# Performance work log

Hardware: AMD Instinct MI355X
Metric: run time of the kernel (lower is better)

The kernel has to match this reference:

```python
import jax, jax.numpy as jnp
import numpy as np
import math

B, S, D, H = 8, 512, 1024, 16
HD = D // H  # 64
FF = 4 * D
EPS = 1e-5


def setup_inputs() -> dict:
    key = jax.random.key(0)
    ks = jax.random.split(key, 12)
    sc = 0.02
    return {
        "x":   jax.random.normal(ks[0], (B, S, D), jnp.float32),
        "Wq":  jax.random.normal(ks[1], (H, D, HD), jnp.float32) * sc,
        "Wk":  jax.random.normal(ks[2], (H, D, HD), jnp.float32) * sc,
        "Wv":  jax.random.normal(ks[3], (H, D, HD), jnp.float32) * sc,
        "Wo":  jax.random.normal(ks[4], (D, D), jnp.float32) * sc,
        "bo":  jnp.zeros((D,), jnp.float32),
        "g1":  jnp.ones((D,), jnp.float32),
        "b1":  jnp.zeros((D,), jnp.float32),
        "g2":  jnp.ones((D,), jnp.float32),
        "b2":  jnp.zeros((D,), jnp.float32),
        "W1":  jax.random.normal(ks[5], (D, FF), jnp.float32) * sc,
        "bf1": jnp.zeros((FF,), jnp.float32),
        "W2":  jax.random.normal(ks[6], (FF, D), jnp.float32) * sc,
        "bf2": jnp.zeros((D,), jnp.float32),
    }


def _layernorm(x, gamma, beta):
    # biased variance, matches torch.var(correction=0)
    mean = jnp.mean(x, axis=-1, keepdims=True)
    var = jnp.mean((x - mean) ** 2, axis=-1, keepdims=True)
    return (x - mean) / jnp.sqrt(var + EPS) * gamma + beta


def _block(x, Wq, Wk, Wv, Wo, bo, g1, b1, g2, b2, W1, bf1, W2, bf2):
    h = _layernorm(x, g1, b1)
    # per-head projections (no bias): [B,H,S,HD]
    Q = jnp.einsum("bsd,hde->bhse", h, Wq)
    K = jnp.einsum("bsd,hde->bhse", h, Wk)
    V = jnp.einsum("bsd,hde->bhse", h, Wv)
    scores = jnp.einsum("bhse,bhte->bhst", Q, K) / math.sqrt(HD)
    causal = jnp.triu(jnp.ones((S, S), bool), k=1)  # upper-triangular masked
    scores = jnp.where(causal, jnp.float32(-1e10), scores)
    att = jax.nn.softmax(scores, axis=-1)  # dropout in eval mode = identity
    ctx = jnp.einsum("bhst,bhte->bhse", att, V)
    # concat heads in order -> [B,S,D]
    ctx = ctx.transpose(0, 2, 1, 3).reshape(B, S, D)
    attn_out = ctx @ Wo + bo
    cache = attn_out + x
    h2 = _layernorm(cache, g2, b2)
    ff = jax.nn.gelu(h2 @ W1 + bf1, approximate=False) @ W2 + bf2
    return ff + cache


def reference(x, Wq, Wk, Wv, Wo, bo, g1, b1, g2, b2, W1, bf1, W2, bf2):
    return _block(x, Wq, Wk, Wv, Wo, bo, g1, b1, g2, b2, W1, bf1, W2, bf2)
```

## Files before the change

### kernel.cpp

```cpp
#include <hip/hip_runtime.h>
#include <hip/hip_bf16.h>

typedef __hip_bfloat16 bf16;

#define B_   8
#define S_   512
#define D_   1024
#define H_   16
#define HD_  64
#define FF_  4096
#define ROWS (B_ * S_)

typedef __attribute__((ext_vector_type(8))) unsigned short u16x8;
typedef __attribute__((ext_vector_type(4))) float f32x4;

typedef __attribute__((address_space(1))) const unsigned int GU32;
typedef __attribute__((address_space(3))) unsigned int LU32;
__device__ __forceinline__ void gld16(const void* g, void* l) {
    __builtin_amdgcn_global_load_lds((GU32*)g, (LU32*)l, 16, 0, 0);
}

__device__ __forceinline__ float bf2f(unsigned short u) {
    union { unsigned int i; float f; } v; v.i = ((unsigned int)u) << 16; return v.f;
}
__device__ __forceinline__ unsigned short f2bfu(float f) {
    bf16 h = __float2bfloat16(f);
    return *reinterpret_cast<unsigned short*>(&h);
}
__device__ __forceinline__ float ldsel(const void* p, size_t i, bool f32) {
    return f32 ? ((const float*)p)[i]
               : __bfloat162float(((const bf16*)p)[i]);
}
__device__ __forceinline__ float gelu_exact(float x) {
    return 0.5f * x * (1.f + erff(x * 0.70710678118654752440f));
}

__device__ __forceinline__ void ln_body(const void* x, const void* gam,
                                        const void* bet, bf16* out,
                                        int row, bool xf32, bool pf32) {
    int tid = threadIdx.x;
    size_t rb = (size_t)row * D_;
    float v[4];
#pragma unroll
    for (int i = 0; i < 4; ++i) v[i] = ldsel(x, rb + tid + i * 256, xf32);
    float s  = v[0] + v[1] + v[2] + v[3];
    float s2 = v[0] * v[0] + v[1] * v[1] + v[2] * v[2] + v[3] * v[3];
#pragma unroll
    for (int off = 32; off > 0; off >>= 1) {
        s  += __shfl_down(s, off);
        s2 += __shfl_down(s2, off);
    }
    __shared__ float red[8];
    int wv = tid >> 6, ln = tid & 63;
    if (ln == 0) { red[wv] = s; red[4 + wv] = s2; }
    __syncthreads();
    s  = red[0] + red[1] + red[2] + red[3];
    s2 = red[4] + red[5] + red[6] + red[7];
    float mean = s * (1.f / 1024.f);
    float var  = s2 * (1.f / 1024.f) - mean * mean;
    float rstd = rsqrtf(var + 1e-5f);
#pragma unroll
    for (int i = 0; i < 4; ++i) {
        int c = tid + i * 256;
        float g = ldsel(gam, c, pf32), b = ldsel(bet, c, pf32);
        out[rb + c] = __float2bfloat16((v[i] - mean) * rstd * g + b);
    }
}

__device__ __forceinline__ void transpose_body(
    const void* src, bf16* dst, int bid, int N, int K, int sK, int sH, bool pf32) {
    int tilesN = N >> 6;
    int tn = bid % tilesN, tk = bid / tilesN;
    int n0 = tn * 64, k0 = tk * 64;
    __shared__ float T[64][65];
    int t = threadIdx.x;
    size_t headoff = (size_t)(n0 >> 6) * sH;
#pragma unroll
    for (int i = 0; i < 16; ++i) {
        int lin = t + i * 256;
        int kl = lin >> 6, nl = lin & 63;
        size_t e = headoff + (size_t)(k0 + kl) * sK + nl;
        T[kl][nl] = ldsel(src, e, pf32);
    }
    __syncthreads();
#pragma unroll
    for (int i = 0; i < 16; ++i) {
        int lin = t + i * 256;
        int nl = lin >> 6, kl = lin & 63;
        dst[(size_t)(n0 + nl) * K + k0 + kl] = __float2bfloat16(T[kl][nl]);
    }
}

__global__ __launch_bounds__(256) void transpose_kernel(
    const void* __restrict__ src, bf16* __restrict__ dst,
    int N, int K, int sK, int sH,
    const unsigned short* __restrict__ probe) {
    transpose_body(src, dst, blockIdx.x, N, K, sK, sH, probe[0] == 0);
}

__global__ __launch_bounds__(256) void prep1_kernel(
    const void* __restrict__ Wq, const void* __restrict__ Wk,
    const void* __restrict__ Wv, const void* __restrict__ Wo,
    const void* __restrict__ x, const void* __restrict__ g1,
    const void* __restrict__ b1,
    bf16* __restrict__ WqT, bf16* __restrict__ WoT, bf16* __restrict__ h,
    const unsigned short* __restrict__ probe) {
    bool pf32 = (probe[0] == 0);
    int bid = blockIdx.x;
    if (bid < 768) {
        int which = bid >> 8;
        const void* src = (which == 0) ? Wq : ((which == 1) ? Wk : Wv);
        transpose_body(src, WqT + (size_t)which * 1024 * 1024, bid & 255,
                       1024, 1024, HD_, D_ * HD_, pf32);
    } else if (bid < 1024) {
        transpose_body(Wo, WoT, bid - 768, 1024, 1024, 1024, 64, pf32);
    } else {
        ln_body(x, g1, b1, h, bid - 1024, pf32, pf32);
    }
}

__global__ __launch_bounds__(256) void prep2_kernel(
    const void* __restrict__ W1, const void* __restrict__ cache_,
    const void* __restrict__ g2, const void* __restrict__ b2,
    bf16* __restrict__ W1T, bf16* __restrict__ h2,
    const unsigned short* __restrict__ probe) {
    bool pf32 = (probe[0] == 0);
    int bid = blockIdx.x;
    if (bid < 1024) transpose_body(W1, W1T, bid, 4096, 1024, FF_, 64, pf32);
    else            ln_body(cache_, g2, b2, h2, bid - 1024, false, pf32);
}

template<int BN>
__global__ __launch_bounds__(256) void gemm_mfma(
    const bf16* __restrict__ A, const bf16* __restrict__ Bt,
    int K, int nSeg, int segShift, size_t segStride,
    const void* __restrict__ bias,
    const void* __restrict__ resid, int resid_ws,
    bf16* __restrict__ outWS, void* __restrict__ outFinal, int mode,
    const unsigned short* __restrict__ probe) {
    constexpr int BM     = 128;
    constexpr int NR     = BN / 32;
    constexpr int PLANES = (BN == 64) ? 2 : 1;
    constexpr int KSTEP  = 32 * PLANES;
    constexpr int CPP    = 8 + BN / 16;
    constexpr int NCH    = PLANES * CPP / 4;
    constexpr int APL    = BM * 32;
    constexpr int BPL    = BN * 32;
    constexpr int AREG   = 2 * PLANES * APL;
    constexpr int STG    = 2 * PLANES * (BM + BN) * 32;
    constexpr int SMEMSZ = (BM * BN > STG) ? (BM * BN) : STG;
    bool pf32 = (probe[0] == 0);
    __shared__ alignas(16) unsigned short SMEM[SMEMSZ];
    int tid  = threadIdx.x;
    int lane = tid & 63, wv = tid >> 6;
    int g = lane >> 4, i16 = lane & 15;
    int wrow = wv >> 1, wcol = wv & 1;

    int GX = gridDim.x, GY = gridDim.y;
    int T = GX * GY;
    int bid = blockIdx.y * GX + blockIdx.x;
    int bm, bn;
    if (((T & 7) == 0) && ((GY & 3) == 0) && ((GX & 1) == 0)) {
        int x = bid & 7, rank = bid >> 3;
        int xr = x >> 1, xc = x & 1;
        int MS = GY >> 2, NS = GX >> 1;
        int G = (NS % 8 == 0) ? 8 : ((NS % 6 == 0) ? 6 : NS);
        int ng = rank / (MS * G);
        int rem = rank - ng * (MS * G);
        int mloc = rem / G, nloc = ng * G + (rem - (rem / G) * G);
        bm = xr * MS + mloc; bn = xc * NS + nloc;
    } else { bm = blockIdx.y; bn = blockIdx.x; }
    int m0 = bm * BM, n0 = bn * BN;

    f32x4 acc[4][NR];
#pragma unroll
    for (int i = 0; i < 4; ++i)
#pragma unroll
        for (int j = 0; j < NR; ++j) acc[i][j] = (f32x4){0.f, 0.f, 0.f, 0.f};

    const unsigned short* gsrc[NCH];
    unsigned short* l0[NCH];
    unsigned short* l1[NCH];
    {
        int rl = lane >> 2, kq = (lane & 3) * 8;
#pragma unroll
        for (int c0 = 0; c0 < NCH; ++c0) {
            int c = c0 * 4 + wv;
            int pl = c / CPP, cc = c - pl * CPP;
            if (cc < 8) {
                gsrc[c0] = (const unsigned short*)A
                         + (size_t)(m0 + cc * 16 + rl) * K + pl * 32 + kq;
                l0[c0] = &SMEM[(0 * PLANES + pl) * APL + cc * 512];
                l1[c0] = &SMEM[(1 * PLANES + pl) * APL + cc * 512];
            } else {
                gsrc[c0] = (const unsigned short*)Bt
                         + (size_t)(n0 + (cc - 8) * 16 + rl) * K + pl * 32 + kq;
                l0[c0] = &SMEM[AREG + (0 * PLANES + pl) * BPL + (cc - 8) * 512];
                l1[c0] = &SMEM[AREG + (1 * PLANES + pl) * BPL + (cc - 8) * 512];
            }
        }
    }

#define STAGE0(KOFF) { _Pragma("unroll") \
    for (int c0 = 0; c0 < NCH; ++c0) gld16(gsrc[c0] + (KOFF), l0[c0]); }
#define STAGE1(KOFF) { _Pragma("unroll") \
    for (int c0 = 0; c0 < NCH; ++c0) gld16(gsrc[c0] + (KOFF), l1[c0]); }
#define COMPUTE(BUF) { \
    _Pragma("unroll") \
    for (int pl = 0; pl < PLANES; ++pl) { \
        u16x8 af[4], bfv[NR]; \
        _Pragma("unroll") \
        for (int i = 0; i < 4; ++i) \
            af[i] = *reinterpret_cast<const u16x8*>( \
                &SMEM[((BUF) * PLANES + pl) * APL + (wrow * 64 + i * 16 + i16) * 32 + g * 8]); \
        _Pragma("unroll") \
        for (int j = 0; j < NR; ++j) \
            bfv[j] = *reinterpret_cast<const u16x8*>( \
                &SMEM[AREG + ((BUF) * PLANES + pl) * BPL + (wcol * (BN / 2) + j * 16 + i16) * 32 + g * 8]); \
        _Pragma("unroll") \
        for (int i = 0; i < 4; ++i) \
            _Pragma("unroll") \
            for (int j = 0; j < NR; ++j) \
                asm("v_mfma_f32_16x16x32_bf16 %0, %1, %2, %0" \
                    : "+v"(acc[i][j]) : "v"(af[i]), "v"(bfv[j])); \
    } }

    STAGE0(0);
    __syncthreads();
    for (int k0 = 0; k0 < K; k0 += 2 * KSTEP) {
        STAGE1(k0 + KSTEP);
        COMPUTE(0);
        __syncthreads();
        if (k0 + 2 * KSTEP < K) STAGE0(k0 + 2 * KSTEP);
        COMPUTE(1);
        __syncthreads();
    }
#undef STAGE0
#undef STAGE1
#undef COMPUTE

    __builtin_amdgcn_sched_barrier(0);
    asm volatile("s_nop 7\n\ts_nop 7\n\ts_nop 7" ::: );
    __builtin_amdgcn_sched_barrier(0);

    if (outFinal && pf32) {
        int coll = i16, rowl = g * 4;
#pragma unroll
        for (int j = 0; j < NR; ++j) {
            int n = n0 + wcol * (BN / 2) + j * 16 + coll;
            int nl = n & (nSeg - 1);
            float bval = (mode != 0) ? ldsel(bias, nl, pf32) : 0.f;
#pragma unroll
            for (int i = 0; i < 4; ++i) {
                int mb = m0 + wrow * 64 + i * 16 + rowl;
#pragma unroll
                for (int r = 0; r < 4; ++r) {
                    size_t idx = (size_t)(mb + r) * nSeg + nl;
                    float c = acc[i][j][r];
                    if (mode == 1) {
                        c += bval;
                        c += resid_ws ? __bfloat162float(((const bf16*)resid)[idx])
                                      : ldsel(resid, idx, pf32);
                    } else if (mode == 2) {
                        c = gelu_exact(c + bval);
                    }
                    ((float*)outFinal)[idx] = c;
                }
            }
        }
    } else {
        unsigned short* Cs = SMEM;
        int seg = n0 >> segShift;
        int nl0 = n0 & (nSeg - 1);
        bf16* dst = outFinal ? (bf16*)outFinal
                             : outWS + (size_t)seg * segStride;
#pragma unroll
        for (int j = 0; j < NR; ++j) {
            int nloc = wcol * (BN / 2) + j * 16 + i16;
            int nl = nl0 + nloc;
            float bval = (mode != 0) ? ldsel(bias, nl, pf32) : 0.f;
#pragma unroll
            for (int i = 0; i < 4; ++i) {
#pragma unroll
                for (int r = 0; r < 4; ++r) {
                    int mloc = wrow * 64 + i * 16 + g * 4 + r;
                    float c = acc[i][j][r];
                    if (mode == 1) {
                        size_t idx = (size_t)(m0 + mloc) * nSeg + nl;
                        c += bval;
                        c += resid_ws ? __bfloat162float(((const bf16*)resid)[idx])
                                      : ldsel(resid, idx, pf32);
                    } else if (mode == 2) {
                        c = gelu_exact(c + bval);
                    }
                    int swzC = ((((mloc >> 2) & 3) ^ (mloc & 3)) << 4);
                    Cs[mloc * BN + (nloc ^ swzC)] = f2bfu(c);
                }
            }
        }
        __syncthreads();
        constexpr int NP = (BM * BN) / 2048;
#pragma unroll
        for (int p = 0; p < NP; ++p) {
            int lin = p * 2048 + tid * 8;
            int m = lin / BN, nn = lin % BN;
            int swzC = ((((m >> 2) & 3) ^ (m & 3)) << 4);
            u16x8 v = *reinterpret_cast<const u16x8*>(&Cs[m * BN + (nn ^ swzC)]);
            *reinterpret_cast<u16x8*>(dst + (size_t)(m0 + m) * nSeg + nl0 + nn) = v;
        }
    }
}

__global__ __launch_bounds__(256) void attn_kernel(const bf16* __restrict__ Qg,
                                                   const bf16* __restrict__ Kg,
                                                   const bf16* __restrict__ Vg,
                                                   bf16* __restrict__ Og) {
    constexpr int P = 72;
    __shared__ alignas(16) unsigned short Ks[64 * P];
    __shared__ alignas(16) unsigned short Vt[64 * P];
    __shared__ alignas(16) unsigned short Ps[64 * P];
    int qb = blockIdx.x;
    int bh = blockIdx.y;
    int b = bh >> 4, h = bh & 15;
    int tid = threadIdx.x;
    int lane = tid & 63, wv = tid >> 6;
    int g = lane >> 4, i16 = lane & 15;
    size_t base = ((size_t)b * S_) * D_ + h * HD_;

    u16x8 qa[2];
    {
        const unsigned short* qp = (const unsigned short*)Qg + base
            + (size_t)(qb * 64 + wv * 16 + i16) * D_ + g * 8;
#pragma unroll
        for (int kk = 0; kk < 2; ++kk) {
            u16x8 v = *reinterpret_cast<const u16x8*>(qp + kk * 32);
#pragma unroll
            for (int e = 0; e < 8; ++e) v[e] = f2bfu(bf2f(v[e]) * 0.125f);
            qa[kk] = v;
        }
    }
    f32x4 ov[4];
#pragma unroll
    for (int dj = 0; dj < 4; ++dj) ov[dj] = (f32x4){0.f, 0.f, 0.f, 0.f};
    float mrow[4], lrow[4];
#pragma unroll
    for (int r = 0; r < 4; ++r) { mrow[r] = -1e30f; lrow[r] = 0.f; }

    int st = tid >> 2, sd = (tid & 3) * 16;
    const unsigned short* Kp = (const unsigned short*)Kg + base + (size_t)st * D_ + sd;
    const unsigned short* Vp = (const unsigned short*)Vg + base + (size_t)st * D_ + sd;
    unsigned short* KsW = &Ks[st * P + sd];
    unsigned short* VtW = &Vt[sd * P + (st ^ sd)];
    int g1 = g >> 1, g0 = g & 1;
    unsigned short* PsW = &Ps[(wv * 16 + g * 4) * P + (i16 ^ (g0 << 3))];
    const unsigned short* PsR = &Ps[(wv * 16 + i16) * P + ((g ^ ((i16 >> 2) & 3)) << 3)];

    for (int kb = 0; kb <= qb; ++kb) {
        __syncthreads();
        size_t ko = (size_t)kb * 64 * D_;
        u16x8 k0 = *reinterpret_cast<const u16x8*>(Kp + ko);
        u16x8 k1 = *reinterpret_cast<const u16x8*>(Kp + ko + 8);
        u16x8 v0 = *reinterpret_cast<const u16x8*>(Vp + ko);
        u16x8 v1 = *reinterpret_cast<const u16x8*>(Vp + ko + 8);
        *reinterpret_cast<u16x8*>(KsW)     = k0;
        *reinterpret_cast<u16x8*>(KsW + 8) = k1;
#pragma unroll
        for (int ii = 0; ii < 8; ++ii) VtW[ii * P] = v0[ii];
#pragma unroll
        for (int ii = 0; ii < 8; ++ii) VtW[(ii + 8) * P] = v1[ii];
        __syncthreads();

        f32x4 sc[4];
#pragma unroll
        for (int tj = 0; tj < 4; ++tj) sc[tj] = (f32x4){0.f, 0.f, 0.f, 0.f};
#pragma unroll
        for (int kk = 0; kk < 2; ++kk)
#pragma unroll
            for (int tj = 0; tj < 4; ++tj) {
                u16x8 kf = *reinterpret_cast<const u16x8*>(
                    &Ks[(tj * 16 + i16) * P + kk * 32 + g * 8]);
                asm("v_mfma_f32_16x16x32_bf16 %0, %1, %2, %0"
                    : "+v"(sc[tj]) : "v"(qa[kk]), "v"(kf));
            }
        __builtin_amdgcn_sched_barrier(0);
        asm volatile("s_nop 7\n\ts_nop 7\n\ts_nop 7" ::: );
        __builtin_amdgcn_sched_barrier(0);

        if (kb == qb) {
#pragma unroll
            for (int tj = 0; tj < 4; ++tj)
#pragma unroll
                for (int r = 0; r < 4; ++r)
                    if (tj * 16 + i16 > wv * 16 + g * 4 + r) sc[tj][r] = -1e30f;
        }
        float al[4];
#pragma unroll
        for (int r = 0; r < 4; ++r) {
            float mt = fmaxf(fmaxf(sc[0][r], sc[1][r]), fmaxf(sc[2][r], sc[3][r]));
            mt = fmaxf(mt, __shfl_xor(mt, 1));
            mt = fmaxf(mt, __shfl_xor(mt, 2));
            mt = fmaxf(mt, __shfl_xor(mt, 4));
            mt = fmaxf(mt, __shfl_xor(mt, 8));
            float mnew = fmaxf(mrow[r], mt);
            al[r] = __expf(mrow[r] - mnew);
            mrow[r] = mnew;
        }
        float psum[4] = {0.f, 0.f, 0.f, 0.f};
        unsigned short pw[4][4];
#pragma unroll
        for (int tj = 0; tj < 4; ++tj)
#pragma unroll
            for (int r = 0; r < 4; ++r) {
                float p = __expf(sc[tj][r] - mrow[r]);
                unsigned short pb = f2bfu(p);
                pw[tj][r] = pb;
                psum[r] += bf2f(pb);
            }
#pragma unroll
        for (int r = 0; r < 4; ++r) {
            float ps = psum[r];
            ps += __shfl_xor(ps, 1);
            ps += __shfl_xor(ps, 2);
            ps += __shfl_xor(ps, 4);
            ps += __shfl_xor(ps, 8);
            lrow[r] = lrow[r] * al[r] + ps;
        }
#pragma unroll
        for (int dj = 0; dj < 4; ++dj)
#pragma unroll
            for (int r = 0; r < 4; ++r) ov[dj][r] *= al[r];
#pragma unroll
        for (int r = 0; r < 4; ++r)
#pragma unroll
            for (int tj = 0; tj < 4; ++tj)
                PsW[r * P + ((tj ^ g1) << 4)] = pw[tj][r];
#pragma unroll
        for (int kk = 0; kk < 2; ++kk) {
            u16x8 pf = *reinterpret_cast<const u16x8*>(PsR + kk * 32);
#pragma unroll
            for (int dj = 0; dj < 4; ++dj) {
                int tcol = ((kk << 5) | (g << 3)) ^ (dj << 4);
                u16x8 vf = *reinterpret_cast<const u16x8*>(
                    &Vt[(dj * 16 + i16) * P + tcol]);
                asm("v_mfma_f32_16x16x32_bf16 %0, %1, %2, %0"
                    : "+v"(ov[dj]) : "v"(pf), "v"(vf));
            }
        }
    }
    __builtin_amdgcn_sched_barrier(0);
    asm volatile("s_nop 7\n\ts_nop 7\n\ts_nop 7" ::: );
    __builtin_amdgcn_sched_barrier(0);
    float rl[4];
#pragma unroll
    for (int r = 0; r < 4; ++r) rl[r] = 1.f / lrow[r];
    bf16* op = Og + base + (size_t)(qb * 64 + wv * 16 + g * 4) * D_ + i16;
#pragma unroll
    for (int r = 0; r < 4; ++r)
#pragma unroll
        for (int dj = 0; dj < 4; ++dj)
            op[(size_t)r * D_ + dj * 16] = __float2bfloat16(ov[dj][r] * rl[r]);
}

extern "C" void kernel_launch(void* const* d_in, const int* in_sizes, int n_in,
                              void* d_out, int out_size, void* d_ws, size_t ws_size,
                              hipStream_t stream) {
    const void* x   = d_in[0];
    const void* Wq  = d_in[1];
    const void* Wk  = d_in[2];
    const void* Wv  = d_in[3];
    const void* Wo  = d_in[4];
    const void* bo  = d_in[5];
    const void* g1  = d_in[6];
    const void* b1  = d_in[7];
    const void* g2  = d_in[8];
    const void* b2  = d_in[9];
    const void* W1  = d_in[10];
    const void* bf1 = d_in[11];
    const void* W2  = d_in[12];
    const void* bf2 = d_in[13];
    const unsigned short* probe = (const unsigned short*)g1;

    bf16* ws = (bf16*)d_ws;
    const size_t Mi = (size_t)1024 * 1024;
    bf16* h     = ws;
    bf16* Qb    = ws + 4 * Mi;
    bf16* Kb    = ws + 8 * Mi;
    bf16* Vb    = ws + 12 * Mi;
    bf16* ctx   = ws;
    bf16* cache = ws + 4 * Mi;
    bf16* h2    = ws + 8 * Mi;
    bf16* ff1   = ws + 12 * Mi;
    bf16* WqT   = ws + 16 * Mi;
    bf16* WoT   = ws + 19 * Mi;
    bf16* W1T   = ws;
    bf16* W2T   = ws + 8 * Mi;

    prep1_kernel<<<5120, 256, 0, stream>>>(Wq, Wk, Wv, Wo, x, g1, b1,
                                           WqT, WoT, h, probe);
    gemm_mfma<128><<<dim3(3072 / 128, ROWS / 128), 256, 0, stream>>>(
        h, WqT, 1024, 1024, 10, 4 * Mi,
        nullptr, nullptr, 0, Qb, nullptr, 0, probe);
    dim3 gA(S_ / 64, B_ * H_);
    attn_kernel<<<gA, 256, 0, stream>>>(Qb, Kb, Vb, ctx);
    gemm_mfma<64><<<dim3(1024 / 64, ROWS / 128), 256, 0, stream>>>(
        ctx, WoT, 1024, 1024, 30, 0,
        bo, x, 0, cache, nullptr, 1, probe);
    prep2_kernel<<<5120, 256, 0, stream>>>(W1, cache, g2, b2, W1T, h2, probe);
    gemm_mfma<128><<<dim3(4096 / 128, ROWS / 128), 256, 0, stream>>>(
        h2, W1T, 1024, 4096, 30, 0,
        bf1, nullptr, 0, ff1, nullptr, 2, probe);
    transpose_kernel<<<1024, 256, 0, stream>>>(W2, W2T, 1024, 4096, 1024, 64, probe);
    gemm_mfma<64><<<dim3(1024 / 64, ROWS / 128), 256, 0, stream>>>(
        ff1, W2T, 4096, 1024, 30, 0,
        bf2, cache, 1, nullptr, d_out, 1, probe);
}
```

Baseline: 359.8 us.

## Templatize GEMM tile height and wave count; prefetch K/V in attention

The GEMM kernel gains template parameters for the M tile size and the wave count. The FF1 GEMM now runs with 256-row tiles on 8 waves (512 threads) to increase reuse of the B operand per block. Separately, the attention kernel loads the next K/V tile into registers during the current iteration, so global load latency overlaps with compute. The larger tile uses more LDS and registers, which may lower occupancy, and the smaller grid leaves fewer blocks to spread across CUs.

Result: no change. 362.7 us (+0.8%).

```diff
diff --git a/kernel.cpp b/kernel.cpp
--- a/kernel.cpp
+++ b/kernel.cpp
@@ -130,20 +130,21 @@
     else            ln_body(cache_, g2, b2, h2, bid - 1024, false, pf32);
 }
 
-template<int BN>
-__global__ __launch_bounds__(256) void gemm_mfma(
+template<int BN, int BM, int NWAVES>
+__global__ __launch_bounds__(NWAVES * 64) void gemm_mfma(
     const bf16* __restrict__ A, const bf16* __restrict__ Bt,
     int K, int nSeg, int segShift, size_t segStride,
     const void* __restrict__ bias,
     const void* __restrict__ resid, int resid_ws,
     bf16* __restrict__ outWS, void* __restrict__ outFinal, int mode,
     const unsigned short* __restrict__ probe) {
-    constexpr int BM     = 128;
+    constexpr int NT     = NWAVES * 64;
     constexpr int NR     = BN / 32;
     constexpr int PLANES = (BN == 64) ? 2 : 1;
     constexpr int KSTEP  = 32 * PLANES;
-    constexpr int CPP    = 8 + BN / 16;
-    constexpr int NCH    = PLANES * CPP / 4;
+    constexpr int ACH    = BM / 16;
+    constexpr int CPP    = ACH + BN / 16;
+    constexpr int NCH    = PLANES * CPP / NWAVES;
     constexpr int APL    = BM * 32;
     constexpr int BPL    = BN * 32;
     constexpr int AREG   = 2 * PLANES * APL;
@@ -185,18 +186,18 @@
         int rl = lane >> 2, kq = (lane & 3) * 8;
 #pragma unroll
         for (int c0 = 0; c0 < NCH; ++c0) {
-            int c = c0 * 4 + wv;
+            int c = c0 * NWAVES + wv;
             int pl = c / CPP, cc = c - pl * CPP;
-            if (cc < 8) {
+            if (cc < ACH) {
                 gsrc[c0] = (const unsigned short*)A
                          + (size_t)(m0 + cc * 16 + rl) * K + pl * 32 + kq;
                 l0[c0] = &SMEM[(0 * PLANES + pl) * APL + cc * 512];
                 l1[c0] = &SMEM[(1 * PLANES + pl) * APL + cc * 512];
             } else {
                 gsrc[c0] = (const unsigned short*)Bt
-                         + (size_t)(n0 + (cc - 8) * 16 + rl) * K + pl * 32 + kq;
-                l0[c0] = &SMEM[AREG + (0 * PLANES + pl) * BPL + (cc - 8) * 512];
-                l1[c0] = &SMEM[AREG + (1 * PLANES + pl) * BPL + (cc - 8) * 512];
+                         + (size_t)(n0 + (cc - ACH) * 16 + rl) * K + pl * 32 + kq;
+                l0[c0] = &SMEM[AREG + (0 * PLANES + pl) * BPL + (cc - ACH) * 512];
+                l1[c0] = &SMEM[AREG + (1 * PLANES + pl) * BPL + (cc - ACH) * 512];
             }
         }
     }
@@ -299,10 +300,10 @@
             }
         }
         __syncthreads();
-        constexpr int NP = (BM * BN) / 2048;
+        constexpr int NP = (BM * BN) / (NT * 8);
 #pragma unroll
         for (int p = 0; p < NP; ++p) {
-            int lin = p * 2048 + tid * 8;
+            int lin = p * (NT * 8) + tid * 8;
             int m = lin / BN, nn = lin % BN;
             int swzC = ((((m >> 2) & 3) ^ (m & 3)) << 4);
             u16x8 v = *reinterpret_cast<const u16x8*>(&Cs[m * BN + (nn ^ swzC)]);
@@ -355,19 +356,26 @@
     unsigned short* PsW = &Ps[(wv * 16 + g * 4) * P + (i16 ^ (g0 << 3))];
     const unsigned short* PsR = &Ps[(wv * 16 + i16) * P + ((g ^ ((i16 >> 2) & 3)) << 3)];
 
+    u16x8 rk0 = *reinterpret_cast<const u16x8*>(Kp);
+    u16x8 rk1 = *reinterpret_cast<const u16x8*>(Kp + 8);
+    u16x8 rv0 = *reinterpret_cast<const u16x8*>(Vp);
+    u16x8 rv1 = *reinterpret_cast<const u16x8*>(Vp + 8);
+
     for (int kb = 0; kb <= qb; ++kb) {
         __syncthreads();
-        size_t ko = (size_t)kb * 64 * D_;
-        u16x8 k0 = *reinterpret_cast<const u16x8*>(Kp + ko);
-        u16x8 k1 = *reinterpret_cast<const u16x8*>(Kp + ko + 8);
-        u16x8 v0 = *reinterpret_cast<const u16x8*>(Vp + ko);
-        u16x8 v1 = *reinterpret_cast<const u16x8*>(Vp + ko + 8);
-        *reinterpret_cast<u16x8*>(KsW)     = k0;
-        *reinterpret_cast<u16x8*>(KsW + 8) = k1;
-#pragma unroll
-        for (int ii = 0; ii < 8; ++ii) VtW[ii * P] = v0[ii];
-#pragma unroll
-        for (int ii = 0; ii < 8; ++ii) VtW[(ii + 8) * P] = v1[ii];
+        *reinterpret_cast<u16x8*>(KsW)     = rk0;
+        *reinterpret_cast<u16x8*>(KsW + 8) = rk1;
+#pragma unroll
+        for (int ii = 0; ii < 8; ++ii) VtW[ii * P] = rv0[ii];
+#pragma unroll
+        for (int ii = 0; ii < 8; ++ii) VtW[(ii + 8) * P] = rv1[ii];
+        if (kb < qb) {
+            size_t ko = (size_t)(kb + 1) * 64 * D_;
+            rk0 = *reinterpret_cast<const u16x8*>(Kp + ko);
+            rk1 = *reinterpret_cast<const u16x8*>(Kp + ko + 8);
+            rv0 = *reinterpret_cast<const u16x8*>(Vp + ko);
+            rv1 = *reinterpret_cast<const u16x8*>(Vp + ko + 8);
+        }
         __syncthreads();
 
         f32x4 sc[4];
@@ -497,20 +505,20 @@
 
     prep1_kernel<<<5120, 256, 0, stream>>>(Wq, Wk, Wv, Wo, x, g1, b1,
                                            WqT, WoT, h, probe);
-    gemm_mfma<128><<<dim3(3072 / 128, ROWS / 128), 256, 0, stream>>>(
+    gemm_mfma<128, 128, 4><<<dim3(3072 / 128, ROWS / 128), 256, 0, stream>>>(
         h, WqT, 1024, 1024, 10, 4 * Mi,
         nullptr, nullptr, 0, Qb, nullptr, 0, probe);
     dim3 gA(S_ / 64, B_ * H_);
     attn_kernel<<<gA, 256, 0, stream>>>(Qb, Kb, Vb, ctx);
-    gemm_mfma<64><<<dim3(1024 / 64, ROWS / 128), 256, 0, stream>>>(
+    gemm_mfma<64, 128, 4><<<dim3(1024 / 64, ROWS / 128), 256, 0, stream>>>(
         ctx, WoT, 1024, 1024, 30, 0,
         bo, x, 0, cache, nullptr, 1, probe);
     prep2_kernel<<<5120, 256, 0, stream>>>(W1, cache, g2, b2, W1T, h2, probe);
-    gemm_mfma<128><<<dim3(4096 / 128, ROWS / 128), 256, 0, stream>>>(
+    gemm_mfma<128, 256, 8><<<dim3(4096 / 128, ROWS / 256), 512, 0, stream>>>(
         h2, W1T, 1024, 4096, 30, 0,
         bf1, nullptr, 0, ff1, nullptr, 2, probe);
     transpose_kernel<<<1024, 256, 0, stream>>>(W2, W2T, 1024, 4096, 1024, 64, probe);
-    gemm_mfma<64><<<dim3(1024 / 64, ROWS / 128), 256, 0, stream>>>(
+    gemm_mfma<64, 128, 4><<<dim3(1024 / 64, ROWS / 128), 256, 0, stream>>>(
         ff1, W2T, 4096, 1024, 30, 0,
         bf2, cache, 1, nullptr, d_out, 1, probe);
 }
```
